# Performance work log

Measured on AMD Instinct MI355X. Metric: run time of the kernel, lower is better.

## Reference

```python
import jax, jax.numpy as jnp
import numpy as np
from jax import lax

B, H_IN, W_IN = 2, 64, 64
C_FEAT = 256
HQ, WQ = 256, 256
HIDDEN_DEPTH = 4
IN_DIM = C_FEAT + 4  # q_feat + rel_coord(2) + rel_cell(2)
OUT_DIM = 2
EPS_SHIFT = 1e-6
CLAMP_EPS = 1e-6


def make_coord(h, w):
    # cell-center coords in [-1,1], dim 0 along H, dim 1 along W (LIIF convention)
    hs = (jnp.arange(h, dtype=jnp.float32) + 0.5) * (2.0 / h) - 1.0
    ws = (jnp.arange(w, dtype=jnp.float32) + 0.5) * (2.0 / w) - 1.0
    return jnp.stack(jnp.meshgrid(hs, ws, indexing='ij'), axis=-1)  # [h,w,2]


def setup_inputs() -> dict:
    key = jax.random.key(0)
    ks = jax.random.split(key, 16)
    inp = jax.random.normal(ks[0], (B, 3, H_IN, W_IN), dtype=jnp.float32)
    coord = jnp.broadcast_to(make_coord(HQ, WQ)[None], (B, HQ, WQ, 2)).astype(jnp.float32)
    cell = jnp.broadcast_to(jnp.array([2.0 / HQ, 2.0 / WQ], dtype=jnp.float32)[None], (B, 2))
    # encoder: single 3x3 conv 3 -> C_FEAT
    conv_w = jax.random.normal(ks[1], (C_FEAT, 3, 3, 3), dtype=jnp.float32) * (1.0 / np.sqrt(3 * 9))
    conv_b = jnp.zeros((C_FEAT,), dtype=jnp.float32)
    # imnet MLP: IN_DIM -> C_FEAT (xHIDDEN_DEPTH, ReLU) -> OUT_DIM
    w_in = jax.random.normal(ks[2], (IN_DIM, C_FEAT), dtype=jnp.float32) * (1.0 / np.sqrt(IN_DIM))
    b_in = jnp.zeros((C_FEAT,), dtype=jnp.float32)
    w_hid = jax.random.normal(ks[3], (HIDDEN_DEPTH - 1, C_FEAT, C_FEAT), dtype=jnp.float32) * (1.0 / np.sqrt(C_FEAT))
    b_hid = jnp.zeros((HIDDEN_DEPTH - 1, C_FEAT), dtype=jnp.float32)
    w_out = jax.random.normal(ks[4], (C_FEAT, OUT_DIM), dtype=jnp.float32) * (1.0 / np.sqrt(C_FEAT))
    b_out = jnp.zeros((OUT_DIM,), dtype=jnp.float32)
    return {"inp": inp, "coord": coord, "cell": cell, "conv_w": conv_w, "conv_b": conv_b,
            "w_in": w_in, "b_in": b_in, "w_hid": w_hid, "b_hid": b_hid,
            "w_out": w_out, "b_out": b_out}


def _mlp(x, w_in, b_in, w_hid, b_hid, w_out, b_out):
    h = jax.nn.relu(x @ w_in + b_in)
    for i in range(w_hid.shape[0]):
        h = jax.nn.relu(h @ w_hid[i] + b_hid[i])
    return h @ w_out + b_out


def _forward(inp, coord, cell, conv_w, conv_b, w_in, b_in, w_hid, b_hid, w_out, b_out):
    feat = lax.conv_general_dilated(inp, conv_w, (1, 1), 'SAME') + conv_b[None, :, None, None]
    Hf, Wf = feat.shape[-2], feat.shape[-1]
    rx = 1.0 / Hf  # 2/H/2
    ry = 1.0 / Wf
    gather = jax.vmap(lambda f, i, j: f[:, i, j])  # [C,H,W],[Hq,Wq]x2 -> [C,Hq,Wq]
    preds, areas = [], []
    for vx in (-1, 1):
        for vy in (-1, 1):
            ch = jnp.clip(coord[..., 0] + vx * rx + EPS_SHIFT, -1 + CLAMP_EPS, 1 - CLAMP_EPS)
            cw = jnp.clip(coord[..., 1] + vy * ry + EPS_SHIFT, -1 + CLAMP_EPS, 1 - CLAMP_EPS)
            # nearest-neighbor grid_sample (align_corners=False): idx = floor((g+1)*size/2)
            ih = jnp.clip(jnp.floor((ch + 1.0) * Hf * 0.5).astype(jnp.int32), 0, Hf - 1)
            iw = jnp.clip(jnp.floor((cw + 1.0) * Wf * 0.5).astype(jnp.int32), 0, Wf - 1)
            q_feat = gather(feat, ih, iw)  # [B,C,Hq,Wq]
            # sampled feat_coord equals cell-center coord of the nearest pixel
            q_ch = (2.0 * ih.astype(jnp.float32) + 1.0) / Hf - 1.0
            q_cw = (2.0 * iw.astype(jnp.float32) + 1.0) / Wf - 1.0
            rel_h = (coord[..., 0] - q_ch) * Hf  # [B,Hq,Wq]
            rel_w = (coord[..., 1] - q_cw) * Wf
            rc_h = jnp.broadcast_to((cell[:, 0] * Hf)[:, None, None], rel_h.shape)
            rc_w = jnp.broadcast_to((cell[:, 1] * Wf)[:, None, None], rel_w.shape)
            x = jnp.concatenate([
                jnp.moveaxis(q_feat, 1, -1),  # [B,Hq,Wq,C]
                rel_h[..., None], rel_w[..., None], rc_h[..., None], rc_w[..., None]
            ], axis=-1)
            preds.append(_mlp(x, w_in, b_in, w_hid, b_hid, w_out, b_out))  # [B,Hq,Wq,2]
            areas.append(jnp.abs(rel_h * rel_w) + 1e-9)
    tot_area = areas[0] + areas[1] + areas[2] + areas[3]
    # local-ensemble diagonal swap
    areas[0], areas[3] = areas[3], areas[0]
    areas[1], areas[2] = areas[2], areas[1]
    ret = sum(p * (a / tot_area)[..., None] for p, a in zip(preds, areas))
    ret = jax.nn.softmax(ret, axis=-1)
    return jnp.moveaxis(ret, -1, 1)  # [B,2,Hq,Wq]


def reference(inp, coord, cell, conv_w, conv_b, w_in, b_in, w_hid, b_hid, w_out, b_out):
    return _forward(inp, coord, cell, conv_w, conv_b, w_in, b_in, w_hid, b_hid, w_out, b_out)
```

## Files before the change

### kernel.cpp

```cpp
#include <hip/hip_runtime.h>

typedef unsigned short ushort_t;
typedef __attribute__((ext_vector_type(8))) _Float16 f16x8;
typedef __attribute__((ext_vector_type(4))) float f32x4;
typedef __attribute__((ext_vector_type(4))) unsigned int u32x4;
typedef __attribute__((ext_vector_type(2))) unsigned long long u64x2;

#define ROWB 576
#define BUFB (64*ROWB)

__device__ __forceinline__ ushort_t f2h(float x){ _Float16 h=(_Float16)x; return __builtin_bit_cast(ushort_t,h); }
__device__ __forceinline__ float h2f(ushort_t u){ return (float)__builtin_bit_cast(_Float16,u); }
__device__ __forceinline__ unsigned int pkrtz(float lo, float hi){
    return __builtin_bit_cast(unsigned int, __builtin_amdgcn_cvt_pkrtz(lo, hi));
}
__device__ __forceinline__ unsigned int pk_add2(unsigned int a, unsigned int b){
    unsigned int r; asm("v_pk_add_f16 %0, %1, %2" : "=v"(r) : "v"(a), "v"(b)); return r;
}
__device__ __forceinline__ unsigned int pk_relu2(unsigned int a){
    unsigned int r; asm("v_pk_max_f16 %0, %1, %2" : "=v"(r) : "v"(a), "v"(0u)); return r;
}

__device__ __forceinline__ int permc(int c){
    return (c & ~31) + (((c >> 2) & 3) << 3) + (c & 3) + (((c >> 4) & 1) << 2);
}

__global__ __launch_bounds__(256) void conv_k(const float* __restrict__ inp,
        const float* __restrict__ w, const float* __restrict__ bias,
        ushort_t* __restrict__ feat)
{
    __shared__ float sw_[6912];
    __shared__ float patch[27];
    int t = threadIdx.x;
    int b = blockIdx.x >> 12, p = blockIdx.x & 4095;
    int y = p >> 6, x = p & 63;
    for (int i = t; i < 6912; i += 256) sw_[i] = w[i];
    if (t < 27){
        int ci = t/9, r = t%9, dy = r/3, dx = r%3;
        int yy = y+dy-1, xx = x+dx-1;
        patch[t] = (yy>=0 && yy<64 && xx>=0 && xx<64) ? inp[((b*3+ci)<<12)+(yy<<6)+xx] : 0.f;
    }
    __syncthreads();
    float acc = bias[t];
    #pragma unroll
    for (int j = 0; j < 27; ++j) acc += patch[j]*sw_[t*27+j];
    feat[(((b<<12)+p)<<8) + permc(t)] = f2h(acc);
}

__global__ __launch_bounds__(256) void pack_k(const float* __restrict__ w_in,
        const float* __restrict__ w_hid, ushort_t* __restrict__ packW)
{
    int i = blockIdx.x*256 + threadIdx.x;
    if (i >= 270336) return;
    int layer, rem;
    if (i < 73728){ layer = 0; rem = i; }
    else { int j = i - 73728; layer = 1 + (j >> 16); rem = j & 65535; }
    int j8 = rem & 7, frag = rem >> 3;
    int lane = frag & 63, kt = frag >> 6;
    int kc = kt >> 4, nt = kt & 15;
    int k = kc*32 + ((lane>>4)<<2) + (j8 & 3) + ((j8 >> 2) << 4);
    int n = (nt<<4) + (lane & 15);
    float val;
    if (layer == 0) val = (k < 260) ? w_in[k*256 + n] : 0.f;
    else            val = w_hid[((layer-1)*256 + k)*256 + n];
    packW[i] = f2h(val);
}

__global__ __launch_bounds__(256) void l0pre_k(const ushort_t* feat,
        const ushort_t* __restrict__ packW, ushort_t* h0)
{
    __shared__ __align__(16) char buf[BUFB];
    const int t = threadIdx.x, lane = t & 63, wave = t >> 6;
    const int b = blockIdx.x >> 6, p0 = (blockIdx.x & 63) << 6;
    {
        int m = t >> 2, q = t & 3;
        char* drow = buf + m*ROWB;
        int sw = ((m & 7) << 4) ^ (q << 4);
        const u64x2* src = (const u64x2*)(feat + (((b<<12) + p0 + m)<<8) + q*64);
        #pragma unroll
        for (int c = 0; c < 8; ++c)
            *(u64x2*)(drow + ((q*128 + c*16) ^ sw)) = src[c];
    }
    __syncthreads();
    const int l15 = lane & 15, g = lane >> 4;
    const int swz = (l15 & 7) << 4;
    f32x4 acc[4][4];
    #pragma unroll
    for (int nt = 0; nt < 4; ++nt)
        #pragma unroll
        for (int mg = 0; mg < 4; ++mg) acc[mg][nt] = (f32x4){0.f,0.f,0.f,0.f};
    const int lofs = (wave*256 + lane)*8;
    f16x8 wA[4], wB[4], aP0[4], aP1[4];
    #pragma unroll
    for (int nt = 0; nt < 4; ++nt){
        wA[nt] = *(const f16x8*)(packW + lofs + nt*512);
        wB[nt] = *(const f16x8*)(packW + lofs + 8192 + nt*512);
    }
    {
        const int o2 = (g*16) ^ swz;
        #pragma unroll
        for (int mg = 0; mg < 4; ++mg)
            aP0[mg] = *(const f16x8*)(buf + (mg*16 + l15)*ROWB + o2);
    }
    #pragma unroll
    for (int kc = 0; kc < 8; ++kc){
        if (kc + 1 < 8){
            const int o2 = ((kc + 1)*64 + g*16) ^ swz ^ ((((kc + 1) >> 1) & 3) << 4);
            if ((kc & 1) == 0){
                #pragma unroll
                for (int mg = 0; mg < 4; ++mg)
                    aP1[mg] = *(const f16x8*)(buf + (mg*16 + l15)*ROWB + o2);
            } else {
                #pragma unroll
                for (int mg = 0; mg < 4; ++mg)
                    aP0[mg] = *(const f16x8*)(buf + (mg*16 + l15)*ROWB + o2);
            }
        }
        if ((kc & 1) == 0){
            #pragma unroll
            for (int mg = 0; mg < 4; ++mg)
                #pragma unroll
                for (int nt = 0; nt < 4; ++nt)
                    acc[mg][nt] = __builtin_amdgcn_mfma_f32_16x16x32_f16(wA[nt], aP0[mg], acc[mg][nt], 0, 0, 0);
        } else {
            #pragma unroll
            for (int mg = 0; mg < 4; ++mg)
                #pragma unroll
                for (int nt = 0; nt < 4; ++nt)
                    acc[mg][nt] = __builtin_amdgcn_mfma_f32_16x16x32_f16(wB[nt], aP1[mg], acc[mg][nt], 0, 0, 0);
        }
        if (kc + 2 < 8){
            const ushort_t* pf = packW + lofs + (kc + 2)*8192;
            if ((kc & 1) == 0){
                #pragma unroll
                for (int nt = 0; nt < 4; ++nt) wA[nt] = *(const f16x8*)(pf + nt*512);
            } else {
                #pragma unroll
                for (int nt = 0; nt < 4; ++nt) wB[nt] = *(const f16x8*)(pf + nt*512);
            }
        }
    }
    #pragma unroll
    for (int mg = 0; mg < 4; ++mg){
        char* row = (char*)(h0 + (((b<<12) + p0 + mg*16 + l15)<<8));
        #pragma unroll
        for (int i = 0; i < 2; ++i){
            const int kb = 2*wave + i;
            f32x4 a0 = acc[mg][2*i], a1 = acc[mg][2*i + 1];
            u32x4 st;
            st[0] = pkrtz(a0[0], a0[1]);
            st[1] = pkrtz(a0[2], a0[3]);
            st[2] = pkrtz(a1[0], a1[1]);
            st[3] = pkrtz(a1[2], a1[3]);
            *(u32x4*)(row + kb*64 + 16*g) = st;
        }
    }
}

template<int KC, bool HAS_NEXT, bool STORE>
__device__ __forceinline__ void mlp_layer(const ushort_t* __restrict__ wfrag,
        const ushort_t* __restrict__ nextw,
        const float* __restrict__ bias, char* __restrict__ buf,
        int lane, int wave, f16x8 (&wP0)[4], f16x8 (&wP1)[4], f32x4 (&acc)[4][4])
{
    const int l15 = lane & 15, g = lane >> 4;
    const int swz  = (l15 & 7) << 4;
    const int aoffg = g*16;
    #pragma unroll
    for (int nt = 0; nt < 4; ++nt){
        f32x4 bv = *(const f32x4*)(bias + (wave*4 + nt)*16 + 4*g);
        #pragma unroll
        for (int mg = 0; mg < 4; ++mg) acc[mg][nt] = bv;
    }
    const int lofs = (wave*4*64 + lane)*8;
    f16x8 aP0[4], aP1[4];
    {
        const int o2 = aoffg ^ swz;
        #pragma unroll
        for (int mg = 0; mg < 4; ++mg)
            aP0[mg] = *(const f16x8*)(buf + (mg*16 + l15)*ROWB + o2);
    }
    #pragma unroll
    for (int kc = 0; kc < KC; ++kc){
        const ushort_t* pfw = nullptr;
        if (kc + 2 < KC)   pfw = wfrag + lofs + (kc + 2)*8192;
        else if (HAS_NEXT) pfw = nextw + lofs + (kc + 2 - KC)*8192;
        const bool la = (kc + 1 < KC);
        if (la){
            const int o2 = ((kc + 1)*64 + aoffg) ^ swz ^ ((((kc + 1) >> 1) & 3) << 4);
            if ((kc & 1) == 0){
                #pragma unroll
                for (int mg = 0; mg < 4; ++mg)
                    aP1[mg] = *(const f16x8*)(buf + (mg*16 + l15)*ROWB + o2);
            } else {
                #pragma unroll
                for (int mg = 0; mg < 4; ++mg)
                    aP0[mg] = *(const f16x8*)(buf + (mg*16 + l15)*ROWB + o2);
            }
        }
        __builtin_amdgcn_s_setprio(1);
        if ((kc & 1) == 0){
            #pragma unroll
            for (int mg = 0; mg < 4; ++mg)
                #pragma unroll
                for (int nt = 0; nt < 4; ++nt)
                    acc[mg][nt] = __builtin_amdgcn_mfma_f32_16x16x32_f16(wP0[nt], aP0[mg], acc[mg][nt], 0, 0, 0);
        } else {
            #pragma unroll
            for (int mg = 0; mg < 4; ++mg)
                #pragma unroll
                for (int nt = 0; nt < 4; ++nt)
                    acc[mg][nt] = __builtin_amdgcn_mfma_f32_16x16x32_f16(wP1[nt], aP1[mg], acc[mg][nt], 0, 0, 0);
        }
        __builtin_amdgcn_s_setprio(0);
        if (pfw){
            if ((kc & 1) == 0){
                #pragma unroll
                for (int nt = 0; nt < 4; ++nt) wP0[nt] = *(const f16x8*)(pfw + nt*512);
            } else {
                #pragma unroll
                for (int nt = 0; nt < 4; ++nt) wP1[nt] = *(const f16x8*)(pfw + nt*512);
            }
        }
    }
    __syncthreads();
    if (STORE){
        const int wsw = swz ^ (wave << 4);
        #pragma unroll
        for (int mg = 0; mg < 4; ++mg){
            char* row = buf + (mg*16 + l15)*ROWB;
            #pragma unroll
            for (int i = 0; i < 2; ++i){
                const int kb = 2*wave + i;
                f32x4 a0 = acc[mg][2*i], a1 = acc[mg][2*i + 1];
                u32x4 st;
                st[0] = pk_relu2(pkrtz(a0[0], a0[1]));
                st[1] = pk_relu2(pkrtz(a0[2], a0[3]));
                st[2] = pk_relu2(pkrtz(a1[0], a1[1]));
                st[3] = pk_relu2(pkrtz(a1[2], a1[3]));
                *(u32x4*)(row + ((kb*64 + 16*g) ^ wsw)) = st;
            }
        }
        __syncthreads();
    }
}

__global__ __launch_bounds__(256, 3) void liif_k(
        const float* __restrict__ coord, const float* __restrict__ cell,
        const float* __restrict__ b_in, const float* __restrict__ b_hid,
        const float* __restrict__ w_out, const float* __restrict__ b_out,
        const ushort_t* __restrict__ h0, const ushort_t* __restrict__ packW,
        float2* __restrict__ preds, float* __restrict__ areas)
{
    __shared__ __align__(16) char buf[BUFB];
    const int t = threadIdx.x, lane = t & 63, wave = t >> 6;
    const int bi = blockIdx.x, v = bi & 3;
    const int tile = bi >> 2;
    const int b = tile >> 10, th = (tile >> 5) & 31, tw = tile & 31;

    f16x8 wX[4], wA[4], wB[4];
    const ushort_t* L1 = packW + 73728;
    {
        const int lofs = (wave*256 + lane)*8;
        #pragma unroll
        for (int nt = 0; nt < 4; ++nt){
            wX[nt] = *(const f16x8*)(packW + 65536 + lofs + nt*512);
            wA[nt] = *(const f16x8*)(L1 + lofs + nt*512);
            wB[nt] = *(const f16x8*)(L1 + 8192 + lofs + nt*512);
        }
    }

    {
        int m = t >> 2, q = t & 3;
        int qh = th*8 + (m >> 3), qw = tw*8 + (m & 7);
        int cidx = (((b<<8) + qh)<<8) + qw;
        float c0 = coord[cidx*2], c1 = coord[cidx*2 + 1];
        float ch = c0 + ((v & 2) ? 0.015625f : -0.015625f); ch = ch + 1e-6f;
        ch = fminf(fmaxf(ch, -1.f + 1e-6f), 1.f - 1e-6f);
        float cw = c1 + ((v & 1) ? 0.015625f : -0.015625f); cw = cw + 1e-6f;
        cw = fminf(fmaxf(cw, -1.f + 1e-6f), 1.f - 1e-6f);
        int ih = (int)floorf((ch + 1.f)*64.f*0.5f); ih = ih < 0 ? 0 : (ih > 63 ? 63 : ih);
        int iw = (int)floorf((cw + 1.f)*64.f*0.5f); iw = iw < 0 ? 0 : (iw > 63 ? 63 : iw);
        char* drow = buf + m*ROWB;
        int sw = ((m & 7) << 4) ^ (q << 4);
        const u64x2* src = (const u64x2*)(h0 + ((((b<<6) + ih)<<6) + iw)*256 + q*64);
        #pragma unroll
        for (int c = 0; c < 8; ++c)
            *(u64x2*)(drow + ((q*128 + c*16) ^ sw)) = src[c];
        if (q == 0){
            float qch = (2.f*(float)ih + 1.f)*(1.f/64.f) - 1.f;
            float qcw = (2.f*(float)iw + 1.f)*(1.f/64.f) - 1.f;
            float relh = (c0 - qch)*64.f, relw = (c1 - qcw)*64.f;
            float rch = cell[b*2]*64.f, rcw = cell[b*2 + 1]*64.f;
            unsigned long long ex = (unsigned long long)f2h(relh)
                | ((unsigned long long)f2h(relw) << 16)
                | ((unsigned long long)f2h(rch)  << 32)
                | ((unsigned long long)f2h(rcw)  << 48);
            u64x2 e; e[0] = ex; e[1] = 0;
            u64x2 z; z[0] = 0;  z[1] = 0;
            int sw2 = (m & 3) << 4;
            #pragma unroll
            for (int c = 1; c < 4; ++c)
                *(u64x2*)(drow + 512 + ((c*16) ^ sw2)) = z;
            *(u64x2*)(drow + 512 + sw2) = e;
            areas[((v*2 + b)<<16) + (qh<<8) + qw] = fabsf(relh*relw) + 1e-9f;
        }
    }
    __syncthreads();

    f32x4 acc[4][4];
    {
        const int l15 = lane & 15, g = lane >> 4;
        const int swz  = (l15 & 7) << 4;
        const int swz2 = (l15 & 3) << 4;
        const int wsw  = swz ^ (wave << 4);
        #pragma unroll
        for (int nt = 0; nt < 4; ++nt){
            f32x4 bv = *(const f32x4*)(b_in + (wave*4 + nt)*16 + 4*g);
            #pragma unroll
            for (int mg = 0; mg < 4; ++mg) acc[mg][nt] = bv;
        }
        f16x8 af[4];
        {
            const int o2 = 512 + ((g*16) ^ swz2);
            #pragma unroll
            for (int mg = 0; mg < 4; ++mg)
                af[mg] = *(const f16x8*)(buf + (mg*16 + l15)*ROWB + o2);
        }
        #pragma unroll
        for (int mg = 0; mg < 4; ++mg)
            #pragma unroll
            for (int nt = 0; nt < 4; ++nt)
                acc[mg][nt] = __builtin_amdgcn_mfma_f32_16x16x32_f16(wX[nt], af[mg], acc[mg][nt], 0, 0, 0);
        #pragma unroll
        for (int mg = 0; mg < 4; ++mg){
            char* row = buf + (mg*16 + l15)*ROWB;
            #pragma unroll
            for (int i = 0; i < 2; ++i){
                const int kb = 2*wave + i;
                u32x4 hv = *(const u32x4*)(row + ((kb*64 + 16*g) ^ wsw));
                f32x4 a0 = acc[mg][2*i], a1 = acc[mg][2*i + 1];
                u32x4 st;
                st[0] = pk_relu2(pk_add2(pkrtz(a0[0], a0[1]), hv[0]));
                st[1] = pk_relu2(pk_add2(pkrtz(a0[2], a0[3]), hv[1]));
                st[2] = pk_relu2(pk_add2(pkrtz(a1[0], a1[1]), hv[2]));
                st[3] = pk_relu2(pk_add2(pkrtz(a1[2], a1[3]), hv[3]));
                *(u32x4*)(row + ((kb*64 + 16*g) ^ wsw)) = st;
            }
        }
        __syncthreads();
    }

    const ushort_t* L2 = packW + 73728 + 65536;
    const ushort_t* L3 = packW + 73728 + 131072;
    mlp_layer<8, true , true >(L1, L2,      b_hid,       buf, lane, wave, wA, wB, acc);
    mlp_layer<8, true , true >(L2, L3,      b_hid + 256, buf, lane, wave, wA, wB, acc);
    mlp_layer<8, false, false>(L3, nullptr, b_hid + 512, buf, lane, wave, wA, wB, acc);

    {
        const int l15 = lane & 15, g = lane >> 4;
        float s0[4] = {0.f,0.f,0.f,0.f}, s1[4] = {0.f,0.f,0.f,0.f};
        #pragma unroll
        for (int j = 0; j < 4; ++j){
            int nb = wave*64 + j*16 + 4*g;
            f32x4 w01 = *(const f32x4*)(w_out + nb*2);
            f32x4 w23 = *(const f32x4*)(w_out + nb*2 + 4);
            #pragma unroll
            for (int mg = 0; mg < 4; ++mg){
                float v0 = fmaxf(acc[mg][j][0], 0.f);
                float v1 = fmaxf(acc[mg][j][1], 0.f);
                float v2 = fmaxf(acc[mg][j][2], 0.f);
                float v3 = fmaxf(acc[mg][j][3], 0.f);
                s0[mg] += v0*w01[0] + v1*w01[2] + v2*w23[0] + v3*w23[2];
                s1[mg] += v0*w01[1] + v1*w01[3] + v2*w23[1] + v3*w23[3];
            }
        }
        float2* stage = (float2*)buf;
        #pragma unroll
        for (int mg = 0; mg < 4; ++mg){
            s0[mg] += __shfl_xor(s0[mg], 16); s0[mg] += __shfl_xor(s0[mg], 32);
            s1[mg] += __shfl_xor(s1[mg], 16); s1[mg] += __shfl_xor(s1[mg], 32);
            if (lane < 16){
                float2 pr; pr.x = s0[mg]; pr.y = s1[mg];
                stage[wave*64 + mg*16 + l15] = pr;
            }
        }
        __syncthreads();
        if (t < 64){
            float2 p0 = stage[t], p1 = stage[64 + t], p2 = stage[128 + t], p3 = stage[192 + t];
            float2 pr;
            pr.x = p0.x + p1.x + p2.x + p3.x + b_out[0];
            pr.y = p0.y + p1.y + p2.y + p3.y + b_out[1];
            int qh = th*8 + (t >> 3), qw = tw*8 + (t & 7);
            preds[((v*2 + b)<<16) + (qh<<8) + qw] = pr;
        }
    }
}

__global__ __launch_bounds__(256) void comb_k(const float2* __restrict__ preds,
        const float* __restrict__ areas, float* __restrict__ out)
{
    int idx = blockIdx.x*256 + threadIdx.x;
    int b = idx >> 16, pix = idx & 65535;
    float a[4]; float2 p[4];
    #pragma unroll
    for (int v = 0; v < 4; ++v){
        int base = ((v*2 + b)<<16) + pix;
        a[v] = areas[base]; p[v] = preds[base];
    }
    float tot = a[0] + a[1] + a[2] + a[3];
    float w0 = a[3]/tot, w1 = a[2]/tot, w2 = a[1]/tot, w3 = a[0]/tot;
    float r0 = p[0].x*w0 + p[1].x*w1 + p[2].x*w2 + p[3].x*w3;
    float r1 = p[0].y*w0 + p[1].y*w1 + p[2].y*w2 + p[3].y*w3;
    float mx = fmaxf(r0, r1);
    float e0 = expf(r0 - mx), e1 = expf(r1 - mx);
    float inv = 1.f/(e0 + e1);
    out[(b<<17) + pix]         = e0*inv;
    out[(b<<17) + 65536 + pix] = e1*inv;
}

extern "C" void kernel_launch(void* const* d_in, const int* in_sizes, int n_in,
                              void* d_out, int out_size, void* d_ws, size_t ws_size,
                              hipStream_t stream)
{
    const float* inp   = (const float*)d_in[0];
    const float* coord = (const float*)d_in[1];
    const float* cell  = (const float*)d_in[2];
    const float* convw = (const float*)d_in[3];
    const float* convb = (const float*)d_in[4];
    const float* w_in  = (const float*)d_in[5];
    const float* b_in  = (const float*)d_in[6];
    const float* w_hid = (const float*)d_in[7];
    const float* b_hid = (const float*)d_in[8];
    const float* w_out = (const float*)d_in[9];
    const float* b_out = (const float*)d_in[10];
    (void)in_sizes; (void)n_in; (void)out_size; (void)ws_size;

    char* ws = (char*)d_ws;
    ushort_t* feat  = (ushort_t*)ws;
    ushort_t* packW = (ushort_t*)(ws + 4194304);
    float2*   preds = (float2*)(ws + 4194304 + 540672);
    float*    areas = (float*)(ws + 4194304 + 540672 + 4194304);
    float* out = (float*)d_out;

    pack_k<<<dim3(1056), dim3(256), 0, stream>>>(w_in, w_hid, packW);
    conv_k<<<dim3(8192), dim3(256), 0, stream>>>(inp, convw, convb, feat);
    l0pre_k<<<dim3(128), dim3(256), 0, stream>>>(feat, packW, feat);
    liif_k<<<dim3(8192), dim3(256), 0, stream>>>(coord, cell, b_in, b_hid,
                                                 w_out, b_out, feat, packW, preds, areas);
    comb_k<<<dim3(512), dim3(256), 0, stream>>>(preds, areas, out);
}
```

Measured before the change: 256.6 us.

## Fuse local-ensemble combine and softmax into the LIIF MLP kernel

Each block's 64 rows now hold 16 query pixels times 4 ensemble shifts instead of 64 pixels for one shift. The area-weighted combine and the 2-way softmax can then run in-block from shared memory. This removes the preds/areas workspace round-trip and the separate comb_k launch. In exchange each block does a little more serial work and an extra barrier, and gathers of the same feature row for neighbouring shifts now land in the same block.

```diff
diff --git a/kernel.cpp b/kernel.cpp
--- a/kernel.cpp
+++ b/kernel.cpp
@@ -250,13 +250,15 @@
         const float* __restrict__ b_in, const float* __restrict__ b_hid,
         const float* __restrict__ w_out, const float* __restrict__ b_out,
         const ushort_t* __restrict__ h0, const ushort_t* __restrict__ packW,
-        float2* __restrict__ preds, float* __restrict__ areas)
+        float* __restrict__ out)
 {
     __shared__ __align__(16) char buf[BUFB];
+    __shared__ float sarea[64];
     const int t = threadIdx.x, lane = t & 63, wave = t >> 6;
-    const int bi = blockIdx.x, v = bi & 3;
-    const int tile = bi >> 2;
-    const int b = tile >> 10, th = (tile >> 5) & 31, tw = tile & 31;
+    const int bi = blockIdx.x;
+    const int b = bi >> 12;
+    const int t12 = bi & 4095;
+    const int th = t12 >> 6, tw = t12 & 63;
 
     f16x8 wX[4], wA[4], wB[4];
     const ushort_t* L1 = packW + 73728;
@@ -266,13 +268,14 @@
         for (int nt = 0; nt < 4; ++nt){
             wX[nt] = *(const f16x8*)(packW + 65536 + lofs + nt*512);
             wA[nt] = *(const f16x8*)(L1 + lofs + nt*512);
-            wB[nt] = *(const f16x8*)(L1 + 8192 + lofs + nt*512);
+            wB[nt] = *(const f16x8*)(L1 + 8192 + nt*512 + lofs);
         }
     }
 
     {
         int m = t >> 2, q = t & 3;
-        int qh = th*8 + (m >> 3), qw = tw*8 + (m & 7);
+        int v = m >> 4, pix = m & 15;
+        int qh = th*4 + (pix >> 2), qw = tw*4 + (pix & 3);
         int cidx = (((b<<8) + qh)<<8) + qw;
         float c0 = coord[cidx*2], c1 = coord[cidx*2 + 1];
         float ch = c0 + ((v & 2) ? 0.015625f : -0.015625f); ch = ch + 1e-6f;
@@ -303,7 +306,7 @@
             for (int c = 1; c < 4; ++c)
                 *(u64x2*)(drow + 512 + ((c*16) ^ sw2)) = z;
             *(u64x2*)(drow + 512 + sw2) = e;
-            areas[((v*2 + b)<<16) + (qh<<8) + qw] = fabsf(relh*relw) + 1e-9f;
+            sarea[m] = fabsf(relh*relw) + 1e-9f;
         }
     }
     __syncthreads();
@@ -375,7 +378,8 @@
                 s1[mg] += v0*w01[1] + v1*w01[3] + v2*w23[1] + v3*w23[3];
             }
         }
-        float2* stage = (float2*)buf;
+        float2* stage  = (float2*)buf;
+        float2* stage2 = (float2*)(buf + 2048);
         #pragma unroll
         for (int mg = 0; mg < 4; ++mg){
             s0[mg] += __shfl_xor(s0[mg], 16); s0[mg] += __shfl_xor(s0[mg], 32);
@@ -389,34 +393,31 @@
         if (t < 64){
             float2 p0 = stage[t], p1 = stage[64 + t], p2 = stage[128 + t], p3 = stage[192 + t];
             float2 pr;
-            pr.x = p0.x + p1.x + p2.x + p3.x + b_out[0];
-            pr.y = p0.y + p1.y + p2.y + p3.y + b_out[1];
-            int qh = th*8 + (t >> 3), qw = tw*8 + (t & 7);
-            preds[((v*2 + b)<<16) + (qh<<8) + qw] = pr;
-        }
-    }
-}
-
-__global__ __launch_bounds__(256) void comb_k(const float2* __restrict__ preds,
-        const float* __restrict__ areas, float* __restrict__ out)
-{
-    int idx = blockIdx.x*256 + threadIdx.x;
-    int b = idx >> 16, pix = idx & 65535;
-    float a[4]; float2 p[4];
-    #pragma unroll
-    for (int v = 0; v < 4; ++v){
-        int base = ((v*2 + b)<<16) + pix;
-        a[v] = areas[base]; p[v] = preds[base];
-    }
-    float tot = a[0] + a[1] + a[2] + a[3];
-    float w0 = a[3]/tot, w1 = a[2]/tot, w2 = a[1]/tot, w3 = a[0]/tot;
-    float r0 = p[0].x*w0 + p[1].x*w1 + p[2].x*w2 + p[3].x*w3;
-    float r1 = p[0].y*w0 + p[1].y*w1 + p[2].y*w2 + p[3].y*w3;
-    float mx = fmaxf(r0, r1);
-    float e0 = expf(r0 - mx), e1 = expf(r1 - mx);
-    float inv = 1.f/(e0 + e1);
-    out[(b<<17) + pix]         = e0*inv;
-    out[(b<<17) + 65536 + pix] = e1*inv;
+            pr.x = p0.x + p1.x + p2.x + p3.x;
+            pr.y = p0.y + p1.y + p2.y + p3.y;
+            stage2[t] = pr;
+        }
+        __syncthreads();
+        if (t < 16){
+            float2 pv[4]; float a[4];
+            #pragma unroll
+            for (int v = 0; v < 4; ++v){
+                pv[v] = stage2[v*16 + t];
+                a[v]  = sarea[v*16 + t];
+            }
+            float tot = a[0] + a[1] + a[2] + a[3];
+            float w0 = a[3]/tot, w1 = a[2]/tot, w2 = a[1]/tot, w3 = a[0]/tot;
+            float r0 = pv[0].x*w0 + pv[1].x*w1 + pv[2].x*w2 + pv[3].x*w3 + b_out[0];
+            float r1 = pv[0].y*w0 + pv[1].y*w1 + pv[2].y*w2 + pv[3].y*w3 + b_out[1];
+            float mx = fmaxf(r0, r1);
+            float e0 = expf(r0 - mx), e1 = expf(r1 - mx);
+            float inv = 1.f/(e0 + e1);
+            int qh = th*4 + (t >> 2), qw = tw*4 + (t & 3);
+            int qidx = (qh << 8) + qw;
+            out[(b<<17) + qidx]         = e0*inv;
+            out[(b<<17) + 65536 + qidx] = e1*inv;
+        }
+    }
 }
 
 extern "C" void kernel_launch(void* const* d_in, const int* in_sizes, int n_in,
@@ -439,14 +440,11 @@
     char* ws = (char*)d_ws;
     ushort_t* feat  = (ushort_t*)ws;
     ushort_t* packW = (ushort_t*)(ws + 4194304);
-    float2*   preds = (float2*)(ws + 4194304 + 540672);
-    float*    areas = (float*)(ws + 4194304 + 540672 + 4194304);
     float* out = (float*)d_out;
 
     pack_k<<<dim3(1056), dim3(256), 0, stream>>>(w_in, w_hid, packW);
     conv_k<<<dim3(8192), dim3(256), 0, stream>>>(inp, convw, convb, feat);
     l0pre_k<<<dim3(128), dim3(256), 0, stream>>>(feat, packW, feat);
     liif_k<<<dim3(8192), dim3(256), 0, stream>>>(coord, cell, b_in, b_hid,
-                                                 w_out, b_out, feat, packW, preds, areas);
-    comb_k<<<dim3(512), dim3(256), 0, stream>>>(preds, areas, out);
-}
+                                                 w_out, b_out, feat, packW, out);
+}
```

After: 258.1 us. About the same (+0.6%).
